# Kernel tuning notes

Measured on AMD Instinct MI355X. Metric: run time of the kernel, lower is better.

## Reference

```python
import jax, jax.numpy as jnp
import numpy as np


def setup_inputs() -> dict:
    key = jax.random.key(0)
    k1, k2 = jax.random.split(key)
    x = jax.random.normal(k1, (8, 2500, 100), dtype=jnp.float32)          # [B, L, E]
    label_feature = jax.random.normal(k2, (8922, 100), dtype=jnp.float32)  # [N, E]
    return {"x": x, "label_feature": label_feature}


def reference(x, label_feature):
    # scores: [B, N, L] = label_feature @ x^T (broadcast query over batch), unscaled
    scores = jnp.einsum("ne,ble->bnl", label_feature, x)
    alpha = jax.nn.softmax(scores, axis=2)  # softmax over sequence length
    # m: [B, N, E] = alpha @ x
    m = jnp.einsum("bnl,ble->bne", alpha, x)
    return m
```

## Files before the change

kernel.cpp:

```cpp
#include <hip/hip_runtime.h>
#include <math.h>
#include <stdint.h>

typedef __attribute__((ext_vector_type(8))) _Float16 half8;
typedef __attribute__((ext_vector_type(4))) _Float16 half4;
typedef __attribute__((ext_vector_type(4))) float f32x4;

constexpr int Bb = 8, Ll = 2500, Ee = 100, Nn = 8922;
constexpr int LP = 2560, EP = 128, NP = 8960;
constexpr int LT = 64;
constexpr int NTILES = LP / LT;
constexpr int NTB = 128;

constexpr size_t SZ_LF = (size_t)NP * EP * 2;
constexpr size_t SZ_XW = (size_t)Bb * LP * EP * 2;
constexpr size_t OFF_XW = SZ_LF;
constexpr size_t OFF_XT = OFF_XW + SZ_XW;
constexpr size_t WS_NEED = OFF_XT + SZ_XW;

__device__ __forceinline__ void gload16(const void* g, void* l) {
    __builtin_amdgcn_global_load_lds(
        (const __attribute__((address_space(1))) uint32_t*)g,
        (__attribute__((address_space(3))) uint32_t*)l, 16, 0, 0);
}

__global__ __launch_bounds__(256)
void prep_lf(const float* __restrict__ lf, uint32_t* __restrict__ dst) {
    int idx = blockIdx.x * 256 + threadIdx.x;
    int n = idx >> 6, ep = idx & 63;
    int e0 = 2 * ep, e1 = e0 + 1;
    float f0 = (n < Nn && e0 < Ee) ? lf[(size_t)n * Ee + e0] : 0.f;
    float f1 = (n < Nn && e1 < Ee) ? lf[(size_t)n * Ee + e1] : (e1 == 127 ? 1.0f : 0.f);
    union { _Float16 h[2]; uint32_t u; } cv;
    cv.h[0] = (_Float16)f0; cv.h[1] = (_Float16)f1;
    dst[idx] = cv.u;
}

__global__ __launch_bounds__(256)
void prep_xw(const float* __restrict__ x, uint32_t* __restrict__ dst) {
    int idx = blockIdx.x * 256 + threadIdx.x;
    int row = idx >> 6, ep = idx & 63;
    int b = row / LP, l = row - b * LP;
    int e0 = 2 * ep, e1 = e0 + 1;
    const size_t src = ((size_t)b * Ll + l) * Ee;
    float f0 = (l < Ll && e0 < Ee) ? x[src + e0] : 0.f;
    float f1;
    if (e1 < Ee)       f1 = (l < Ll) ? x[src + e1] : 0.f;
    else if (e1 == 127) f1 = (l < Ll) ? 0.f : -20000.f;
    else               f1 = 0.f;
    union { _Float16 h[2]; uint32_t u; } cv;
    cv.h[0] = (_Float16)f0; cv.h[1] = (_Float16)f1;
    int boff = (4 * ep) ^ ((l & 7) << 4);
    dst[(size_t)row * 64 + (boff >> 2)] = cv.u;
}

__global__ __launch_bounds__(256)
void prep_xt(const float* __restrict__ x, uint16_t* __restrict__ dst) {
    __shared__ float lx[LT][101];
    int l0 = blockIdx.x * LT;
    int b  = blockIdx.y;
    for (int i = threadIdx.x; i < LT * Ee; i += 256) {
        int ll = i / Ee, e = i - ll * Ee;
        int l = l0 + ll;
        lx[ll][e] = (l < Ll) ? x[((size_t)b * Ll + l) * Ee + e] : 0.f;
    }
    __syncthreads();
    for (int i = threadIdx.x; i < EP * LT; i += 256) {
        int e = i >> 6, ll = i & 63;
        float v = (e < Ee) ? lx[ll][e] : 0.f;
        uint32_t boff = (uint32_t)((2 * ll) ^ ((e & 7) << 4));
        union { _Float16 h; uint16_t u; } cv; cv.h = (_Float16)v;
        dst[((size_t)b * EP + e) * LP + l0 + (boff >> 1)] = cv.u;
    }
}

__global__ __launch_bounds__(512)
void cwa_mfma(const uint16_t* __restrict__ lf16, const uint16_t* __restrict__ xw,
              const uint16_t* __restrict__ xt, float* __restrict__ out) {
    __shared__ __align__(128) char smem[2 * 32768 + 8 * 2048];
    const int tid = threadIdx.x, lane = tid & 63, w = tid >> 6;
    const int g = lane >> 4, nl = lane & 15;
    const int b = blockIdx.y;
    const int n_base = blockIdx.x * NTB + w * 16;

    half8 qf[4];
    {
        const uint16_t* qr = lf16 + (size_t)(n_base + nl) * EP + 8 * g;
#pragma unroll
        for (int ks = 0; ks < 4; ks++) qf[ks] = *(const half8*)(qr + 32 * ks);
    }

    f32x4 oacc[7];
#pragma unroll
    for (int es = 0; es < 7; es++) oacc[es] = f32x4{0.f, 0.f, 0.f, 0.f};
    float m_i = -INFINITY, s_i = 0.f;

    const char* xwb = (const char*)(xw + (size_t)b * LP * EP);
    const char* xtb = (const char*)(xt + (size_t)b * EP * LP);

    {
        char* kb = smem; char* vb = smem + 16384;
#pragma unroll
        for (int i = 0; i < 2; i++) {
            int uo = i * 8192 + w * 1024;
            gload16(xwb + uo + lane * 16, kb + uo);
        }
#pragma unroll
        for (int i = 0; i < 2; i++) {
            int e0 = w * 16 + i * 8;
            gload16(xtb + (size_t)(e0 + (lane >> 3)) * (LP * 2) + (lane & 7) * 16,
                    vb + e0 * 128);
        }
    }
    asm volatile("s_waitcnt vmcnt(0)" ::: "memory");
    __syncthreads();

    char* pb = smem + 65536 + w * 2048;
    const int swp = (nl & 7) << 4;

    for (int t = 0; t < NTILES; t++) {
        const int buf = t & 1;
        const char* kb = smem + buf * 32768;
        const char* vb = kb + 16384;

        if (t + 1 < NTILES) {
            char* kb2 = smem + (buf ^ 1) * 32768; char* vb2 = kb2 + 16384;
            const char* kg = xwb + (size_t)(t + 1) * LT * EP * 2;
            const char* vg = xtb + (size_t)(t + 1) * LT * 2;
#pragma unroll
            for (int i = 0; i < 2; i++) {
                int uo = i * 8192 + w * 1024;
                gload16(kg + uo + lane * 16, kb2 + uo);
            }
#pragma unroll
            for (int i = 0; i < 2; i++) {
                int e0 = w * 16 + i * 8;
                gload16(vg + (size_t)(e0 + (lane >> 3)) * (LP * 2) + (lane & 7) * 16,
                        vb2 + e0 * 128);
            }
        }

        f32x4 sacc[4];
#pragma unroll
        for (int ls = 0; ls < 4; ls++) sacc[ls] = f32x4{0.f, 0.f, 0.f, 0.f};
#pragma unroll
        for (int ls = 0; ls < 4; ls++) {
            const int lrow = 16 * ls + nl;
            const char* kr = kb + lrow * 256;
            const int sw = (lrow & 7) << 4;
#pragma unroll
            for (int ks = 0; ks < 4; ks++) {
                half8 kf = *(const half8*)(kr + ((64 * ks + 16 * g) ^ sw));
                sacc[ls] = __builtin_amdgcn_mfma_f32_16x16x32_f16(kf, qf[ks], sacc[ls], 0, 0, 0);
            }
        }

        float tm = -INFINITY;
#pragma unroll
        for (int ls = 0; ls < 4; ls++)
#pragma unroll
            for (int r = 0; r < 4; r++) tm = fmaxf(tm, sacc[ls][r]);
        tm = fmaxf(tm, __shfl_xor(tm, 16, 64));
        tm = fmaxf(tm, __shfl_xor(tm, 32, 64));
        const float mn = fmaxf(m_i, tm);
        const float scale = __expf(m_i - mn);
        float ts = 0.f;
        half4 ph[4];
#pragma unroll
        for (int ls = 0; ls < 4; ls++)
#pragma unroll
            for (int r = 0; r < 4; r++) {
                float pv = __expf(sacc[ls][r] - mn);
                ts += pv;
                ph[ls][r] = (_Float16)pv;
            }
        ts += __shfl_xor(ts, 16, 64);
        ts += __shfl_xor(ts, 32, 64);
        s_i = s_i * scale + ts;
        m_i = mn;

        float scr[4];
#pragma unroll
        for (int r = 0; r < 4; r++) scr[r] = __shfl(scale, 4 * g + r, 64);
#pragma unroll
        for (int es = 0; es < 7; es++)
#pragma unroll
            for (int r = 0; r < 4; r++) oacc[es][r] *= scr[r];

#pragma unroll
        for (int ls = 0; ls < 4; ls++)
            *(half4*)(pb + nl * 128 + ((32 * ls + 8 * g) ^ swp)) = ph[ls];

#pragma unroll
        for (int kl = 0; kl < 2; kl++) {
            half8 pf = *(const half8*)(pb + nl * 128 + ((64 * kl + 16 * g) ^ swp));
#pragma unroll
            for (int es = 0; es < 7; es++) {
                const int er = 16 * es + nl;
                half8 vf = *(const half8*)(vb + er * 128 + ((64 * kl + 16 * g) ^ ((er & 7) << 4)));
                oacc[es] = __builtin_amdgcn_mfma_f32_16x16x32_f16(pf, vf, oacc[es], 0, 0, 0);
            }
        }

        asm volatile("s_waitcnt vmcnt(0)" ::: "memory");
        __syncthreads();
    }

    const float inv = 1.0f / s_i;
    float invr[4];
#pragma unroll
    for (int r = 0; r < 4; r++) invr[r] = __shfl(inv, 4 * g + r, 64);
#pragma unroll
    for (int es = 0; es < 7; es++) {
        const int e = 16 * es + nl;
        if (e < Ee) {
#pragma unroll
            for (int r = 0; r < 4; r++) {
                const int n = n_base + 4 * g + r;
                if (n < Nn) out[((size_t)b * Nn + n) * Ee + e] = oacc[es][r] * invr[r];
            }
        }
    }
}

constexpr int FNT = 16, FLT = 64, FLTP = 65;
__global__ __launch_bounds__(256)
void cwa_fwd(const float* __restrict__ x, const float* __restrict__ lf,
             float* __restrict__ out) {
    __shared__ float q[FNT][Ee];
    __shared__ float xts[Ee][FLTP];
    __shared__ float pl[FNT][FLT];
    const int tid = threadIdx.x, lane = tid & 63, w = tid >> 6;
    const int b = blockIdx.y, n0 = blockIdx.x * FNT;
    for (int idx = tid; idx < FNT * Ee; idx += 256) {
        int nl = idx / Ee, e = idx - nl * Ee;
        int n = n0 + nl;
        q[nl][e] = (n < Nn) ? lf[n * Ee + e] : 0.0f;
    }
    float m_i[4], s_i[4], a0[4], a1[4];
#pragma unroll
    for (int i = 0; i < 4; i++) { m_i[i] = -INFINITY; s_i[i] = 0.f; a0[i] = 0.f; a1[i] = 0.f; }
    const float* xb = x + (size_t)b * Ll * Ee;
    const bool hi_ok = lane < (Ee - 64);
    for (int l0 = 0; l0 < Ll; l0 += FLT) {
        const int nrows = min(FLT, Ll - l0);
        __syncthreads();
        for (int idx = tid; idx < FLT * (Ee / 4); idx += 256) {
            int r = idx / (Ee / 4), c4 = idx - r * (Ee / 4);
            float4 v = make_float4(0.f, 0.f, 0.f, 0.f);
            if (r < nrows) v = *reinterpret_cast<const float4*>(xb + (size_t)(l0 + r) * Ee + c4 * 4);
            xts[c4 * 4 + 0][r] = v.x; xts[c4 * 4 + 1][r] = v.y;
            xts[c4 * 4 + 2][r] = v.z; xts[c4 * 4 + 3][r] = v.w;
        }
        __syncthreads();
        float sc[4] = {0.f, 0.f, 0.f, 0.f};
        for (int e = 0; e < Ee; e++) {
            float xv = xts[e][lane];
#pragma unroll
            for (int i = 0; i < 4; i++) sc[i] = fmaf(q[4 * w + i][e], xv, sc[i]);
        }
        const bool valid = lane < nrows;
#pragma unroll
        for (int i = 0; i < 4; i++) {
            float s = valid ? sc[i] : -INFINITY;
            float tm = s;
#pragma unroll
            for (int msk = 32; msk >= 1; msk >>= 1) tm = fmaxf(tm, __shfl_xor(tm, msk, 64));
            float mn = fmaxf(m_i[i], tm);
            float p = __expf(s - mn);
            float sm = p;
#pragma unroll
            for (int msk = 32; msk >= 1; msk >>= 1) sm += __shfl_xor(sm, msk, 64);
            float scl = __expf(m_i[i] - mn);
            s_i[i] = s_i[i] * scl + sm; m_i[i] = mn;
            a0[i] *= scl; a1[i] *= scl;
            pl[4 * w + i][lane] = p;
        }
        __syncthreads();
#pragma unroll 4
        for (int l = 0; l < FLT; l++) {
            float xv0 = xts[lane][l];
            float xv1 = hi_ok ? xts[64 + lane][l] : 0.f;
#pragma unroll
            for (int i = 0; i < 4; i++) {
                float pv = pl[4 * w + i][l];
                a0[i] = fmaf(pv, xv0, a0[i]); a1[i] = fmaf(pv, xv1, a1[i]);
            }
        }
    }
#pragma unroll
    for (int i = 0; i < 4; i++) {
        int n = n0 + 4 * w + i;
        if (n >= Nn) continue;
        float inv = 1.0f / s_i[i];
        size_t base = ((size_t)b * Nn + n) * Ee;
        out[base + lane] = a0[i] * inv;
        if (hi_ok) out[base + 64 + lane] = a1[i] * inv;
    }
}

extern "C" void kernel_launch(void* const* d_in, const int* in_sizes, int n_in,
                              void* d_out, int out_size, void* d_ws, size_t ws_size,
                              hipStream_t stream) {
    const float* x  = (const float*)d_in[0];
    const float* lf = (const float*)d_in[1];
    float* out = (float*)d_out;
    if (ws_size >= WS_NEED) {
        uint32_t* lf16 = (uint32_t*)d_ws;
        uint32_t* xww  = (uint32_t*)((char*)d_ws + OFF_XW);
        uint16_t* xtw  = (uint16_t*)((char*)d_ws + OFF_XT);
        prep_lf<<<NP * 64 / 256, 256, 0, stream>>>(lf, lf16);
        prep_xw<<<Bb * LP * 64 / 256, 256, 0, stream>>>(x, xww);
        prep_xt<<<dim3(LP / LT, Bb), 256, 0, stream>>>(x, xtw);
        cwa_mfma<<<dim3(NP / NTB, Bb), 512, 0, stream>>>(
            (const uint16_t*)d_ws, (const uint16_t*)((char*)d_ws + OFF_XW),
            (const uint16_t*)((char*)d_ws + OFF_XT), out);
    } else {
        dim3 grid((Nn + FNT - 1) / FNT, Bb);
        cwa_fwd<<<grid, dim3(256), 0, stream>>>(x, lf, out);
    }
}
```

Measured before the change: 270.2 us.

## Process two query row-tiles per wave and fuse x prep kernels

Each wave in the attention kernel now handles 32 label rows (two 16-row halves) instead of 16, so every K and V fragment read from LDS feeds two MFMAs. The block shrinks from 512 to 256 threads, with launch bounds requesting two blocks per CU. The two x-preparation kernels are merged into one that stages x in shared memory once and writes both the row-major and transposed fp16 copies, saving a launch and a second read of x. The cost is higher register pressure from the doubled accumulators, which may limit occupancy, and each wave now issues twice as many global-to-LDS loads per tile.

```diff
diff --git a/kernel.cpp b/kernel.cpp
--- a/kernel.cpp
+++ b/kernel.cpp
@@ -37,85 +37,89 @@
 }
 
 __global__ __launch_bounds__(256)
-void prep_xw(const float* __restrict__ x, uint32_t* __restrict__ dst) {
-    int idx = blockIdx.x * 256 + threadIdx.x;
-    int row = idx >> 6, ep = idx & 63;
-    int b = row / LP, l = row - b * LP;
-    int e0 = 2 * ep, e1 = e0 + 1;
-    const size_t src = ((size_t)b * Ll + l) * Ee;
-    float f0 = (l < Ll && e0 < Ee) ? x[src + e0] : 0.f;
-    float f1;
-    if (e1 < Ee)       f1 = (l < Ll) ? x[src + e1] : 0.f;
-    else if (e1 == 127) f1 = (l < Ll) ? 0.f : -20000.f;
-    else               f1 = 0.f;
-    union { _Float16 h[2]; uint32_t u; } cv;
-    cv.h[0] = (_Float16)f0; cv.h[1] = (_Float16)f1;
-    int boff = (4 * ep) ^ ((l & 7) << 4);
-    dst[(size_t)row * 64 + (boff >> 2)] = cv.u;
-}
-
-__global__ __launch_bounds__(256)
-void prep_xt(const float* __restrict__ x, uint16_t* __restrict__ dst) {
+void prep_x(const float* __restrict__ x, uint32_t* __restrict__ dxw,
+            uint16_t* __restrict__ dxt) {
     __shared__ float lx[LT][101];
-    int l0 = blockIdx.x * LT;
-    int b  = blockIdx.y;
+    const int l0 = blockIdx.x * LT;
+    const int b  = blockIdx.y;
     for (int i = threadIdx.x; i < LT * Ee; i += 256) {
         int ll = i / Ee, e = i - ll * Ee;
         int l = l0 + ll;
         lx[ll][e] = (l < Ll) ? x[((size_t)b * Ll + l) * Ee + e] : 0.f;
     }
     __syncthreads();
+    for (int i = threadIdx.x; i < LT * 64; i += 256) {
+        int row = i >> 6, ep = i & 63;
+        int l = l0 + row;
+        int e0 = 2 * ep, e1 = e0 + 1;
+        float f0 = (e0 < Ee) ? lx[row][e0] : 0.f;
+        float f1;
+        if (e1 < Ee)        f1 = lx[row][e1];
+        else if (e1 == 127) f1 = (l < Ll) ? 0.f : -20000.f;
+        else                f1 = 0.f;
+        union { _Float16 h[2]; uint32_t u; } cv;
+        cv.h[0] = (_Float16)f0; cv.h[1] = (_Float16)f1;
+        int boff = (4 * ep) ^ ((row & 7) << 4);
+        dxw[((size_t)b * LP + l) * 64 + (boff >> 2)] = cv.u;
+    }
     for (int i = threadIdx.x; i < EP * LT; i += 256) {
         int e = i >> 6, ll = i & 63;
         float v = (e < Ee) ? lx[ll][e] : 0.f;
         uint32_t boff = (uint32_t)((2 * ll) ^ ((e & 7) << 4));
         union { _Float16 h; uint16_t u; } cv; cv.h = (_Float16)v;
-        dst[((size_t)b * EP + e) * LP + l0 + (boff >> 1)] = cv.u;
-    }
-}
-
-__global__ __launch_bounds__(512)
+        dxt[((size_t)b * EP + e) * LP + l0 + (boff >> 1)] = cv.u;
+    }
+}
+
+__global__ __launch_bounds__(256, 2)
 void cwa_mfma(const uint16_t* __restrict__ lf16, const uint16_t* __restrict__ xw,
               const uint16_t* __restrict__ xt, float* __restrict__ out) {
-    __shared__ __align__(128) char smem[2 * 32768 + 8 * 2048];
+    __shared__ __align__(128) char smem[2 * 32768 + 4 * 4096];
     const int tid = threadIdx.x, lane = tid & 63, w = tid >> 6;
     const int g = lane >> 4, nl = lane & 15;
     const int b = blockIdx.y;
-    const int n_base = blockIdx.x * NTB + w * 16;
-
-    half8 qf[4];
-    {
-        const uint16_t* qr = lf16 + (size_t)(n_base + nl) * EP + 8 * g;
-#pragma unroll
-        for (int ks = 0; ks < 4; ks++) qf[ks] = *(const half8*)(qr + 32 * ks);
-    }
-
-    f32x4 oacc[7];
-#pragma unroll
-    for (int es = 0; es < 7; es++) oacc[es] = f32x4{0.f, 0.f, 0.f, 0.f};
-    float m_i = -INFINITY, s_i = 0.f;
+    const int n_base = blockIdx.x * NTB + w * 32;
+
+    half8 qf[2][4];
+#pragma unroll
+    for (int nh = 0; nh < 2; nh++) {
+        const uint16_t* qr = lf16 + (size_t)(n_base + 16 * nh + nl) * EP + 8 * g;
+#pragma unroll
+        for (int ks = 0; ks < 4; ks++) qf[nh][ks] = *(const half8*)(qr + 32 * ks);
+    }
+
+    f32x4 oacc[2][7];
+#pragma unroll
+    for (int nh = 0; nh < 2; nh++)
+#pragma unroll
+        for (int es = 0; es < 7; es++) oacc[nh][es] = f32x4{0.f, 0.f, 0.f, 0.f};
+    float m_i[2] = {-INFINITY, -INFINITY}, s_i[2] = {0.f, 0.f};
 
     const char* xwb = (const char*)(xw + (size_t)b * LP * EP);
     const char* xtb = (const char*)(xt + (size_t)b * EP * LP);
 
-    {
-        char* kb = smem; char* vb = smem + 16384;
-#pragma unroll
-        for (int i = 0; i < 2; i++) {
-            int uo = i * 8192 + w * 1024;
-            gload16(xwb + uo + lane * 16, kb + uo);
-        }
-#pragma unroll
-        for (int i = 0; i < 2; i++) {
-            int e0 = w * 16 + i * 8;
-            gload16(xtb + (size_t)(e0 + (lane >> 3)) * (LP * 2) + (lane & 7) * 16,
-                    vb + e0 * 128);
-        }
-    }
+    auto stage = [&](int t, char* kbuf) {
+        const char* kg = xwb + (size_t)t * LT * EP * 2;
+        const char* vg = xtb + (size_t)t * LT * 2;
+        char* vbuf = kbuf + 16384;
+#pragma unroll
+        for (int i = 0; i < 4; i++) {
+            int uo = i * 4096 + w * 1024;
+            gload16(kg + uo + lane * 16, kbuf + uo);
+        }
+#pragma unroll
+        for (int i = 0; i < 4; i++) {
+            int e0 = w * 32 + i * 8;
+            gload16(vg + (size_t)(e0 + (lane >> 3)) * (LP * 2) + (lane & 7) * 16,
+                    vbuf + e0 * 128);
+        }
+    };
+
+    stage(0, smem);
     asm volatile("s_waitcnt vmcnt(0)" ::: "memory");
     __syncthreads();
 
-    char* pb = smem + 65536 + w * 2048;
+    char* pb = smem + 65536 + w * 4096;
     const int swp = (nl & 7) << 4;
 
     for (int t = 0; t < NTILES; t++) {
@@ -123,26 +127,13 @@
         const char* kb = smem + buf * 32768;
         const char* vb = kb + 16384;
 
-        if (t + 1 < NTILES) {
-            char* kb2 = smem + (buf ^ 1) * 32768; char* vb2 = kb2 + 16384;
-            const char* kg = xwb + (size_t)(t + 1) * LT * EP * 2;
-            const char* vg = xtb + (size_t)(t + 1) * LT * 2;
-#pragma unroll
-            for (int i = 0; i < 2; i++) {
-                int uo = i * 8192 + w * 1024;
-                gload16(kg + uo + lane * 16, kb2 + uo);
-            }
-#pragma unroll
-            for (int i = 0; i < 2; i++) {
-                int e0 = w * 16 + i * 8;
-                gload16(vg + (size_t)(e0 + (lane >> 3)) * (LP * 2) + (lane & 7) * 16,
-                        vb2 + e0 * 128);
-            }
-        }
-
-        f32x4 sacc[4];
-#pragma unroll
-        for (int ls = 0; ls < 4; ls++) sacc[ls] = f32x4{0.f, 0.f, 0.f, 0.f};
+        if (t + 1 < NTILES) stage(t + 1, smem + (buf ^ 1) * 32768);
+
+        f32x4 sacc[2][4];
+#pragma unroll
+        for (int nh = 0; nh < 2; nh++)
+#pragma unroll
+            for (int ls = 0; ls < 4; ls++) sacc[nh][ls] = f32x4{0.f, 0.f, 0.f, 0.f};
 #pragma unroll
         for (int ls = 0; ls < 4; ls++) {
             const int lrow = 16 * ls + nl;
@@ -151,54 +142,64 @@
 #pragma unroll
             for (int ks = 0; ks < 4; ks++) {
                 half8 kf = *(const half8*)(kr + ((64 * ks + 16 * g) ^ sw));
-                sacc[ls] = __builtin_amdgcn_mfma_f32_16x16x32_f16(kf, qf[ks], sacc[ls], 0, 0, 0);
-            }
-        }
-
-        float tm = -INFINITY;
-#pragma unroll
-        for (int ls = 0; ls < 4; ls++)
-#pragma unroll
-            for (int r = 0; r < 4; r++) tm = fmaxf(tm, sacc[ls][r]);
-        tm = fmaxf(tm, __shfl_xor(tm, 16, 64));
-        tm = fmaxf(tm, __shfl_xor(tm, 32, 64));
-        const float mn = fmaxf(m_i, tm);
-        const float scale = __expf(m_i - mn);
-        float ts = 0.f;
-        half4 ph[4];
-#pragma unroll
-        for (int ls = 0; ls < 4; ls++)
+                sacc[0][ls] = __builtin_amdgcn_mfma_f32_16x16x32_f16(kf, qf[0][ks], sacc[0][ls], 0, 0, 0);
+                sacc[1][ls] = __builtin_amdgcn_mfma_f32_16x16x32_f16(kf, qf[1][ks], sacc[1][ls], 0, 0, 0);
+            }
+        }
+
+        float scale_s[2];
+        half4 ph[2][4];
+#pragma unroll
+        for (int nh = 0; nh < 2; nh++) {
+            float tm = -INFINITY;
+#pragma unroll
+            for (int ls = 0; ls < 4; ls++)
+#pragma unroll
+                for (int r = 0; r < 4; r++) tm = fmaxf(tm, sacc[nh][ls][r]);
+            tm = fmaxf(tm, __shfl_xor(tm, 16, 64));
+            tm = fmaxf(tm, __shfl_xor(tm, 32, 64));
+            const float mn = fmaxf(m_i[nh], tm);
+            scale_s[nh] = __expf(m_i[nh] - mn);
+            float ts = 0.f;
+#pragma unroll
+            for (int ls = 0; ls < 4; ls++)
+#pragma unroll
+                for (int r = 0; r < 4; r++) {
+                    float pv = __expf(sacc[nh][ls][r] - mn);
+                    ts += pv;
+                    ph[nh][ls][r] = (_Float16)pv;
+                }
+            ts += __shfl_xor(ts, 16, 64);
+            ts += __shfl_xor(ts, 32, 64);
+            s_i[nh] = s_i[nh] * scale_s[nh] + ts;
+            m_i[nh] = mn;
+        }
+
+#pragma unroll
+        for (int nh = 0; nh < 2; nh++)
 #pragma unroll
             for (int r = 0; r < 4; r++) {
-                float pv = __expf(sacc[ls][r] - mn);
-                ts += pv;
-                ph[ls][r] = (_Float16)pv;
-            }
-        ts += __shfl_xor(ts, 16, 64);
-        ts += __shfl_xor(ts, 32, 64);
-        s_i = s_i * scale + ts;
-        m_i = mn;
-
-        float scr[4];
-#pragma unroll
-        for (int r = 0; r < 4; r++) scr[r] = __shfl(scale, 4 * g + r, 64);
-#pragma unroll
-        for (int es = 0; es < 7; es++)
-#pragma unroll
-            for (int r = 0; r < 4; r++) oacc[es][r] *= scr[r];
-
-#pragma unroll
-        for (int ls = 0; ls < 4; ls++)
-            *(half4*)(pb + nl * 128 + ((32 * ls + 8 * g) ^ swp)) = ph[ls];
+                float scr = __shfl(scale_s[nh], 4 * g + r, 64);
+#pragma unroll
+                for (int es = 0; es < 7; es++) oacc[nh][es][r] *= scr;
+            }
+
+#pragma unroll
+        for (int nh = 0; nh < 2; nh++)
+#pragma unroll
+            for (int ls = 0; ls < 4; ls++)
+                *(half4*)(pb + (16 * nh + nl) * 128 + ((32 * ls + 8 * g) ^ swp)) = ph[nh][ls];
 
 #pragma unroll
         for (int kl = 0; kl < 2; kl++) {
-            half8 pf = *(const half8*)(pb + nl * 128 + ((64 * kl + 16 * g) ^ swp));
+            half8 pf0 = *(const half8*)(pb + nl * 128 + ((64 * kl + 16 * g) ^ swp));
+            half8 pf1 = *(const half8*)(pb + (16 + nl) * 128 + ((64 * kl + 16 * g) ^ swp));
 #pragma unroll
             for (int es = 0; es < 7; es++) {
                 const int er = 16 * es + nl;
                 half8 vf = *(const half8*)(vb + er * 128 + ((64 * kl + 16 * g) ^ ((er & 7) << 4)));
-                oacc[es] = __builtin_amdgcn_mfma_f32_16x16x32_f16(pf, vf, oacc[es], 0, 0, 0);
+                oacc[0][es] = __builtin_amdgcn_mfma_f32_16x16x32_f16(pf0, vf, oacc[0][es], 0, 0, 0);
+                oacc[1][es] = __builtin_amdgcn_mfma_f32_16x16x32_f16(pf1, vf, oacc[1][es], 0, 0, 0);
             }
         }
 
@@ -206,18 +207,19 @@
         __syncthreads();
     }
 
-    const float inv = 1.0f / s_i;
-    float invr[4];
-#pragma unroll
-    for (int r = 0; r < 4; r++) invr[r] = __shfl(inv, 4 * g + r, 64);
-#pragma unroll
-    for (int es = 0; es < 7; es++) {
-        const int e = 16 * es + nl;
-        if (e < Ee) {
-#pragma unroll
-            for (int r = 0; r < 4; r++) {
-                const int n = n_base + 4 * g + r;
-                if (n < Nn) out[((size_t)b * Nn + n) * Ee + e] = oacc[es][r] * invr[r];
+#pragma unroll
+    for (int nh = 0; nh < 2; nh++) {
+        const float inv = 1.0f / s_i[nh];
+#pragma unroll
+        for (int r = 0; r < 4; r++) {
+            const float invr = __shfl(inv, 4 * g + r, 64);
+            const int n = n_base + 16 * nh + 4 * g + r;
+            if (n < Nn) {
+#pragma unroll
+                for (int es = 0; es < 7; es++) {
+                    const int e = 16 * es + nl;
+                    if (e < Ee) out[((size_t)b * Nn + n) * Ee + e] = oacc[nh][es][r] * invr;
+                }
             }
         }
     }
@@ -306,13 +308,10 @@
     const float* lf = (const float*)d_in[1];
     float* out = (float*)d_out;
     if (ws_size >= WS_NEED) {
-        uint32_t* lf16 = (uint32_t*)d_ws;
-        uint32_t* xww  = (uint32_t*)((char*)d_ws + OFF_XW);
-        uint16_t* xtw  = (uint16_t*)((char*)d_ws + OFF_XT);
-        prep_lf<<<NP * 64 / 256, 256, 0, stream>>>(lf, lf16);
-        prep_xw<<<Bb * LP * 64 / 256, 256, 0, stream>>>(x, xww);
-        prep_xt<<<dim3(LP / LT, Bb), 256, 0, stream>>>(x, xtw);
-        cwa_mfma<<<dim3(NP / NTB, Bb), 512, 0, stream>>>(
+        prep_lf<<<NP * 64 / 256, 256, 0, stream>>>(lf, (uint32_t*)d_ws);
+        prep_x<<<dim3(LP / LT, Bb), 256, 0, stream>>>(
+            x, (uint32_t*)((char*)d_ws + OFF_XW), (uint16_t*)((char*)d_ws + OFF_XT));
+        cwa_mfma<<<dim3(NP / NTB, Bb), 256, 0, stream>>>(
             (const uint16_t*)d_ws, (const uint16_t*)((char*)d_ws + OFF_XW),
             (const uint16_t*)((char*)d_ws + OFF_XT), out);
     } else {
```

Measured after the change: 248.3 us. 8.1% less time.
